# Performance work log

Hardware: AMD Instinct MI355X
Metric: run time of the kernel (lower is better)

The kernel has to match this reference:

```python
import jax, jax.numpy as jnp
import numpy as np

N_EMBD = 1024
N_HEAD = 16
HEAD_SIZE = N_EMBD // N_HEAD
D_FF = 4 * N_EMBD
B, T = 4, 2048
EPS = 1e-5


def _layernorm(x, w, b):
    mu = jnp.mean(x, axis=-1, keepdims=True)
    var = jnp.mean(jnp.square(x - mu), axis=-1, keepdims=True)
    return (x - mu) * jax.lax.rsqrt(var + EPS) * w + b


def setup_inputs() -> dict:
    key = jax.random.key(0)
    ks = jax.random.split(key, 12)
    s = 0.02
    x = jax.random.normal(ks[0], (B, T, N_EMBD), dtype=jnp.float32)
    # right-padded prefix mask: lengths in [T//2, T] -> no all-masked causal rows
    lengths = jax.random.randint(ks[1], (B,), T // 2, T + 1)
    key_padding_mask = jnp.arange(T)[None, :] < lengths[:, None]  # [B,T] bool, True=keep
    wq = jax.random.normal(ks[2], (N_EMBD, N_HEAD, HEAD_SIZE), dtype=jnp.float32) * s
    wk = jax.random.normal(ks[3], (N_EMBD, N_HEAD, HEAD_SIZE), dtype=jnp.float32) * s
    wv = jax.random.normal(ks[4], (N_EMBD, N_HEAD, HEAD_SIZE), dtype=jnp.float32) * s
    proj_w = jax.random.normal(ks[5], (N_EMBD, N_EMBD), dtype=jnp.float32) * s
    proj_b = jnp.zeros((N_EMBD,), dtype=jnp.float32)
    ff_w1 = jax.random.normal(ks[6], (N_EMBD, D_FF), dtype=jnp.float32) * s
    ff_b1 = jnp.zeros((D_FF,), dtype=jnp.float32)
    ff_w2 = jax.random.normal(ks[7], (D_FF, N_EMBD), dtype=jnp.float32) * s
    ff_b2 = jnp.zeros((N_EMBD,), dtype=jnp.float32)
    ln1_w = jnp.ones((N_EMBD,), dtype=jnp.float32)
    ln1_b = jnp.zeros((N_EMBD,), dtype=jnp.float32)
    ln2_w = jnp.ones((N_EMBD,), dtype=jnp.float32)
    ln2_b = jnp.zeros((N_EMBD,), dtype=jnp.float32)
    return dict(x=x, key_padding_mask=key_padding_mask, wq=wq, wk=wk, wv=wv,
                proj_w=proj_w, proj_b=proj_b, ff_w1=ff_w1, ff_b1=ff_b1,
                ff_w2=ff_w2, ff_b2=ff_b2, ln1_w=ln1_w, ln1_b=ln1_b,
                ln2_w=ln2_w, ln2_b=ln2_b)


def reference(x, key_padding_mask, wq, wk, wv, proj_w, proj_b,
              ff_w1, ff_b1, ff_w2, ff_b2, ln1_w, ln1_b, ln2_w, ln2_b):
    Bn, Tn, C = x.shape
    m = key_padding_mask.astype(x.dtype)  # [B,T]
    # --- attention sublayer ---
    h = _layernorm(x, ln1_w, ln1_b) * m[..., None]
    q = jnp.einsum('btc,chd->bhtd', h, wq)
    k = jnp.einsum('btc,chd->bhtd', h, wk)
    v = jnp.einsum('btc,chd->bhtd', h, wv)
    # NOTE: original scales by full embed dim C**-0.5, not head_size
    scores = jnp.einsum('bhtd,bhsd->bhts', q, k) * (C ** -0.5)
    causal = jnp.tril(jnp.ones((Tn, Tn), dtype=bool))
    mask = causal[None, None, :, :] & key_padding_mask[:, None, None, :]
    scores = jnp.where(mask, scores, -jnp.inf)
    wei = jax.nn.softmax(scores, axis=-1)
    out = jnp.einsum('bhts,bhsd->bthd', wei, v).reshape(Bn, Tn, C)
    x = x + out @ proj_w + proj_b
    # --- feedforward sublayer ---
    h2 = _layernorm(x, ln2_w, ln2_b) * m[..., None]
    ff = jax.nn.relu(h2 @ ff_w1 + ff_b1) @ ff_w2 + ff_b2
    x = (x + ff) * m[..., None]
    return x
```

## Files before the change

### kernel.cpp

```cpp
#include <hip/hip_runtime.h>
#include <math.h>

typedef float f32x4 __attribute__((ext_vector_type(4)));
typedef float f4 __attribute__((ext_vector_type(4)));
typedef __bf16 bf16x8 __attribute__((ext_vector_type(8)));
typedef __bf16 bf16x4 __attribute__((ext_vector_type(4)));

#define GLOBAL_AS __attribute__((address_space(1)))
#define LDS_AS __attribute__((address_space(3)))

__global__ __launch_bounds__(256) void mask_canon(const unsigned char* __restrict__ raw,
                                                  float* __restrict__ msk, int n) {
    int i = blockIdx.x * 256 + threadIdx.x;
    if (i >= n) return;
    unsigned int w0 = *(const unsigned int*)raw;
    float v;
    if (w0 == 0x01010101u)       v = raw[i] ? 1.f : 0.f;
    else if (w0 == 0x3f800000u)  v = ((const float*)raw)[i];
    else                         v = ((const int*)raw)[i] ? 1.f : 0.f;
    msk[i] = v;
}

__global__ __launch_bounds__(256) void lens_kernel(const float* __restrict__ msk,
                                                   float* __restrict__ lens) {
    int b = blockIdx.x, tid = threadIdx.x;
    float s = 0.f;
    for (int i = tid; i < 2048; i += 256) s += msk[b * 2048 + i];
#pragma unroll
    for (int off = 1; off < 64; off <<= 1) s += __shfl_xor(s, off);
    __shared__ float red[4];
    int wave = tid >> 6, lane = tid & 63;
    if (lane == 0) red[wave] = s;
    __syncthreads();
    if (tid == 0) lens[b] = red[0] + red[1] + red[2] + red[3];
}

__global__ __launch_bounds__(256) void tcvt(const float* __restrict__ src,
                                            __bf16* __restrict__ dst, int K, int N) {
    __shared__ float tile[32][33];
    int n0 = blockIdx.x * 32, k0 = blockIdx.y * 32;
    int tx = threadIdx.x & 31, ty = threadIdx.x >> 5;
#pragma unroll
    for (int i = 0; i < 4; ++i)
        tile[ty + 8 * i][tx] = src[(long)(k0 + ty + 8 * i) * N + n0 + tx];
    __syncthreads();
#pragma unroll
    for (int i = 0; i < 4; ++i)
        dst[(long)(n0 + ty + 8 * i) * K + k0 + tx] = (__bf16)tile[tx][ty + 8 * i];
}

__global__ __launch_bounds__(256) void ln_kernel(const float* __restrict__ x,
                                                 const float* __restrict__ w,
                                                 const float* __restrict__ bsc,
                                                 const float* __restrict__ msk,
                                                 __bf16* __restrict__ out) {
    long row = blockIdx.x;
    int tid = threadIdx.x;
    f4 xv = *(const f4*)(x + row * 1024 + tid * 4);
    float s = xv[0] + xv[1] + xv[2] + xv[3];
    float sq = xv[0] * xv[0] + xv[1] * xv[1] + xv[2] * xv[2] + xv[3] * xv[3];
#pragma unroll
    for (int off = 1; off < 64; off <<= 1) {
        s += __shfl_xor(s, off);
        sq += __shfl_xor(sq, off);
    }
    __shared__ float red[2][4];
    int wave = tid >> 6, lane = tid & 63;
    if (lane == 0) { red[0][wave] = s; red[1][wave] = sq; }
    __syncthreads();
    s = red[0][0] + red[0][1] + red[0][2] + red[0][3];
    sq = red[1][0] + red[1][1] + red[1][2] + red[1][3];
    float mu = s * (1.0f / 1024.0f);
    float var = sq * (1.0f / 1024.0f) - mu * mu;
    float rs = rsqrtf(var + 1e-5f);
    float mv = msk[row];
    f4 wv = *(const f4*)(w + tid * 4);
    f4 bv = *(const f4*)(bsc + tid * 4);
    bf16x4 ov;
#pragma unroll
    for (int j = 0; j < 4; ++j)
        ov[j] = (__bf16)(((xv[j] - mu) * rs * wv[j] + bv[j]) * mv);
    *(bf16x4*)(out + row * 1024 + tid * 4) = ov;
}

template <int EP>
__global__ __launch_bounds__(256) void gemm_bt(const __bf16* __restrict__ A,
                                               const __bf16* __restrict__ B,
                                               int K, int N, void* __restrict__ Cout,
                                               const float* __restrict__ bias,
                                               const float* __restrict__ resid,
                                               const float* __restrict__ mskp) {
    __shared__ __bf16 As[128 * 32];
    __shared__ __bf16 Bs[128 * 32];
    int tid = threadIdx.x;
    int wave = tid >> 6, lane = tid & 63;
    int l15 = lane & 15, quad = lane >> 4;
    int wrow = (wave >> 1) * 64, wcol = (wave & 1) * 64;
    long rowBase = (long)blockIdx.x * 128;
    long colBase = (long)blockIdx.y * 128;
    const __bf16* Ab = A + rowBase * K;
    const __bf16* Bb = B + colBase * K;
    int srow = lane >> 2;
    int scol = (lane & 3) * 8;
    f32x4 acc[4][4] = {};

    for (int kt = 0; kt < K; kt += 32) {
#pragma unroll
        for (int j = 0; j < 2; ++j) {
            int seg = wave * 2 + j;
            const __bf16* ga = Ab + (long)(seg * 16 + srow) * K + kt + scol;
            const __bf16* gb = Bb + (long)(seg * 16 + srow) * K + kt + scol;
            __builtin_amdgcn_global_load_lds((const GLOBAL_AS void*)ga,
                                             (LDS_AS void*)((char*)As + seg * 1024), 16, 0, 0);
            __builtin_amdgcn_global_load_lds((const GLOBAL_AS void*)gb,
                                             (LDS_AS void*)((char*)Bs + seg * 1024), 16, 0, 0);
        }
        __syncthreads();
        bf16x8 af[4], bfr[4];
#pragma unroll
        for (int i = 0; i < 4; ++i) {
            af[i] = *(const bf16x8*)(As + (wrow + i * 16 + l15) * 32 + quad * 8);
            bfr[i] = *(const bf16x8*)(Bs + (wcol + i * 16 + l15) * 32 + quad * 8);
        }
#pragma unroll
        for (int mi = 0; mi < 4; ++mi)
#pragma unroll
            for (int ni = 0; ni < 4; ++ni)
                acc[mi][ni] = __builtin_amdgcn_mfma_f32_16x16x32_bf16(af[mi], bfr[ni], acc[mi][ni], 0, 0, 0);
        __syncthreads();
    }

#pragma unroll
    for (int mi = 0; mi < 4; ++mi) {
#pragma unroll
        for (int r = 0; r < 4; ++r) {
            long gr = rowBase + wrow + mi * 16 + quad * 4 + r;
#pragma unroll
            for (int ni = 0; ni < 4; ++ni) {
                long gc = colBase + wcol + ni * 16 + l15;
                float v = acc[mi][ni][r];
                if constexpr (EP == 2) {
                    v += bias[gc] + resid[gr * N + gc];
                    ((float*)Cout)[gr * N + gc] = v;
                } else {
                    v = (v + bias[gc] + resid[gr * N + gc]) * mskp[gr];
                    ((float*)Cout)[gr * N + gc] = v;
                }
            }
        }
    }
}

template <int EP>
__global__ __launch_bounds__(512, 2) void gemm_bt8(const __bf16* __restrict__ A,
                                                   const __bf16* __restrict__ B,
                                                   int K, int N, void* __restrict__ Cout,
                                                   const float* __restrict__ bias) {
    __shared__ __bf16 AB[2][2][256 * 64];
    int tid = threadIdx.x;
    int wave = tid >> 6, lane = tid & 63;
    int l15 = lane & 15, quad = lane >> 4;
    int r8 = l15 & 7;
    int wm = wave >> 2, wn = wave & 3;
    long rowBase = (long)blockIdx.x * 256;
    long colBase = (long)blockIdx.y * 256;
    const __bf16* Ab = A + rowBase * K;
    const __bf16* Bb = B + colBase * K;
    int srow = lane >> 3;
    int scol = ((lane & 7) ^ srow) * 8;
    f32x4 acc[8][4] = {};

#define STAGE2(DST, GB, seg0, kt_)                                                         \
    do {                                                                                   \
        _Pragma("unroll") for (int j = 0; j < 2; ++j) {                                    \
            int s_ = wave * 4 + (seg0) + j;                                                \
            const __bf16* g_ = (GB) + (long)(s_ * 8 + srow) * K + (kt_) + scol;            \
            __builtin_amdgcn_global_load_lds((const GLOBAL_AS void*)g_,                    \
                                             (LDS_AS void*)((char*)(DST) + s_ * 1024), 16, \
                                             0, 0);                                        \
        }                                                                                  \
    } while (0)

#define RDA(mh)                                                                      \
    do {                                                                             \
        _Pragma("unroll") for (int mi = 0; mi < 4; ++mi) {                           \
            int row_ = wm * 128 + (mh) * 64 + mi * 16 + l15;                         \
            af[mi][0] = *(const bf16x8*)(Ac + row_ * 64 + ((quad ^ r8) << 3));       \
            af[mi][1] = *(const bf16x8*)(Ac + row_ * 64 + (((4 + quad) ^ r8) << 3)); \
        }                                                                            \
    } while (0)

#define RDB(h)                                                                              \
    do {                                                                                    \
        _Pragma("unroll") for (int ni = 0; ni < 2; ++ni) {                                  \
            int row_ = wn * 64 + ((h) * 2 + ni) * 16 + l15;                                 \
            bfr[h][ni][0] = *(const bf16x8*)(Bc + row_ * 64 + ((quad ^ r8) << 3));          \
            bfr[h][ni][1] = *(const bf16x8*)(Bc + row_ * 64 + (((4 + quad) ^ r8) << 3));    \
        }                                                                                   \
    } while (0)

#define MM(mh, nh)                                                                          \
    do {                                                                                    \
        __builtin_amdgcn_s_setprio(1);                                                      \
        _Pragma("unroll") for (int mi = 0; mi < 4; ++mi) {                                  \
            _Pragma("unroll") for (int ni = 0; ni < 2; ++ni) {                              \
                acc[(mh) * 4 + mi][(nh) * 2 + ni] = __builtin_amdgcn_mfma_f32_16x16x32_bf16(\
                    af[mi][0], bfr[nh][ni][0], acc[(mh) * 4 + mi][(nh) * 2 + ni], 0, 0, 0); \
                acc[(mh) * 4 + mi][(nh) * 2 + ni] = __builtin_amdgcn_mfma_f32_16x16x32_bf16(\
                    af[mi][1], bfr[nh][ni][1], acc[(mh) * 4 + mi][(nh) * 2 + ni], 0, 0, 0); \
            }                                                                               \
        }                                                                                   \
        __builtin_amdgcn_s_setprio(0);                                                      \
    } while (0)

    STAGE2(&AB[0][0][0], Ab, 0, 0);
    STAGE2(&AB[0][0][0], Ab, 2, 0);
    STAGE2(&AB[0][1][0], Bb, 0, 0);
    STAGE2(&AB[0][1][0], Bb, 2, 0);

    int cur = 0;
    bf16x8 af[4][2], bfr[2][2][2];
    for (int kt = 0; kt < K; kt += 64) {
        const bool lastt = (kt + 64 >= K);
        const __bf16* Ac = &AB[cur][0][0];
        const __bf16* Bc = &AB[cur][1][0];
        __bf16* An = &AB[cur ^ 1][0][0];
        __bf16* Bn = &AB[cur ^ 1][1][0];
        if (!lastt) {
            STAGE2(An, Ab, 0, kt + 64);
            __asm__ volatile("s_waitcnt vmcnt(2)" ::: "memory");
        } else {
            __asm__ volatile("s_waitcnt vmcnt(0)" ::: "memory");
        }
        __asm__ volatile("s_barrier" ::: "memory");
        RDA(0);
        RDB(0);
        MM(0, 0);
        if (!lastt) STAGE2(An, Ab, 2, kt + 64);
        RDB(1);
        MM(0, 1);
        if (!lastt) STAGE2(Bn, Bb, 0, kt + 64);
        RDA(1);
        MM(1, 1);
        if (!lastt) STAGE2(Bn, Bb, 2, kt + 64);
        MM(1, 0);
        __asm__ volatile("s_barrier" ::: "memory");
        cur ^= 1;
    }
#undef STAGE2
#undef RDA
#undef RDB
#undef MM

#pragma unroll
    for (int mi = 0; mi < 8; ++mi) {
#pragma unroll
        for (int r = 0; r < 4; ++r) {
            long gr = rowBase + wm * 128 + mi * 16 + quad * 4 + r;
#pragma unroll
            for (int ni = 0; ni < 4; ++ni) {
                long gc = colBase + wn * 64 + ni * 16 + l15;
                float v = acc[mi][ni][r];
                if constexpr (EP == 0) {
                    ((__bf16*)Cout)[gr * N + gc] = (__bf16)v;
                } else {
                    v += bias[gc];
                    v = v > 0.f ? v : 0.f;
                    ((__bf16*)Cout)[gr * N + gc] = (__bf16)v;
                }
            }
        }
    }
}

#define SWIZ(row, d) ((row) * 64 + ((((d) >> 3) ^ ((row) & 7)) << 3) + ((d) & 7))
__global__ __launch_bounds__(256, 3) void attn_kernel(const __bf16* __restrict__ qkv,
                                                      const float* __restrict__ lens,
                                                      __bf16* __restrict__ att) {
    const int T = 2048, C3 = 3072;
    int bh = blockIdx.x;
    int qt = 15 - blockIdx.y;
    int h = bh & 15, b = bh >> 4;
    int tid = threadIdx.x;
    int wave = tid >> 6, lane = tid & 63, l15 = lane & 15, quad = lane >> 4;

    __shared__ __bf16 Kl[64 * 64];
    __shared__ __bf16 Vt[64 * 64];
    __shared__ __bf16 Pl[4][32 * 64];

    long rowB = (long)b * T;
    const __bf16* kbase = qkv + rowB * C3 + 1024 + h * 64;
    const __bf16* vbase = qkv + rowB * C3 + 2048 + h * 64;
    const float scale2 = (1.0f / 32.0f) * 1.44269504088896f;

    int krow = tid >> 2, kd = (tid & 3) * 16;
    int vk = (tid & 15) * 4, vd = (tid >> 4) * 4;
    int vc8 = vk >> 3, vk7 = vk & 7;

    bf16x8 ones;
#pragma unroll
    for (int j = 0; j < 8; ++j) ones[j] = (__bf16)1.0f;

    __bf16* pw = &Pl[wave][0];
    int r8 = l15 & 7;

    int qbase = qt * 128;
    int wq0 = qbase + wave * 32;

    bf16x8 qf[2][2];
#pragma unroll
    for (int g = 0; g < 2; ++g) {
        const __bf16* qptr = qkv + (rowB + wq0 + g * 16 + l15) * C3 + h * 64;
        qf[g][0] = *(const bf16x8*)(qptr + quad * 8);
        qf[g][1] = *(const bf16x8*)(qptr + 32 + quad * 8);
    }

    f32x4 o0[4] = {}, o1[4] = {};
    f32x4 lacc0 = {}, lacc1 = {};
    int nchunk = 2 * qt + 2;
    float len = lens[b];

    bf16x8 kpre0, kpre1;
    bf16x4 vpre[4];
    {
        const __bf16* kg = kbase + (long)krow * C3 + kd;
        kpre0 = *(const bf16x8*)kg;
        kpre1 = *(const bf16x8*)(kg + 8);
#pragma unroll
        for (int j = 0; j < 4; ++j)
            vpre[j] = *(const bf16x4*)(vbase + (long)(vk + j) * C3 + vd);
    }

    for (int c = 0; c < nchunk; ++c) {
        int k0 = c * 64;
        __asm__ volatile("s_barrier" ::: "memory");
        *(bf16x8*)(&Kl[SWIZ(krow, kd)]) = kpre0;
        *(bf16x8*)(&Kl[SWIZ(krow, kd + 8)]) = kpre1;
#pragma unroll
        for (int dd = 0; dd < 4; ++dd) {
            bf16x4 w = {vpre[0][dd], vpre[1][dd], vpre[2][dd], vpre[3][dd]};
            int d = vd + dd;
            *(bf16x4*)(&Vt[d * 64 + ((vc8 ^ (d & 7)) << 3) + vk7]) = w;
        }
        if (c + 1 < nchunk) {
            int k1 = k0 + 64;
            const __bf16* kg = kbase + (long)(k1 + krow) * C3 + kd;
            kpre0 = *(const bf16x8*)kg;
            kpre1 = *(const bf16x8*)(kg + 8);
#pragma unroll
            for (int j = 0; j < 4; ++j)
                vpre[j] = *(const bf16x4*)(vbase + (long)(k1 + vk + j) * C3 + vd);
        }
        __asm__ volatile("s_waitcnt lgkmcnt(0)\n\ts_barrier" ::: "memory");

        if (k0 <= wq0 + 31) {
            f32x4 s0[4] = {}, s1[4] = {};
#pragma unroll
            for (int n = 0; n < 4; ++n) {
                int row = n * 16 + l15;
                bf16x8 kb0 = *(const bf16x8*)(&Kl[row * 64 + ((quad ^ r8) << 3)]);
                bf16x8 kb1 = *(const bf16x8*)(&Kl[row * 64 + (((4 + quad) ^ r8) << 3)]);
                s0[n] = __builtin_amdgcn_mfma_f32_16x16x32_bf16(kb0, qf[0][0], s0[n], 0, 0, 0);
                s0[n] = __builtin_amdgcn_mfma_f32_16x16x32_bf16(kb1, qf[0][1], s0[n], 0, 0, 0);
                s1[n] = __builtin_amdgcn_mfma_f32_16x16x32_bf16(kb0, qf[1][0], s1[n], 0, 0, 0);
                s1[n] = __builtin_amdgcn_mfma_f32_16x16x32_bf16(kb1, qf[1][1], s1[n], 0, 0, 0);
            }

            bool needC = (k0 + 63 > wq0);
#pragma unroll
            for (int n = 0; n < 4; ++n) {
                int c8 = n * 2 + (quad >> 1);
                int sub = (quad & 1) * 4;
                bf16x4 w0, w1;
                if (!needC) {
#pragma unroll
                    for (int r = 0; r < 4; ++r) {
                        w0[r] = (__bf16)exp2f(s0[n][r] * scale2);
                        w1[r] = (__bf16)exp2f(s1[n][r] * scale2);
                    }
                } else {
                    int kg = k0 + n * 16 + quad * 4;
                    int qg0 = wq0 + l15, qg1 = wq0 + 16 + l15;
#pragma unroll
                    for (int r = 0; r < 4; ++r) {
                        w0[r] = (kg + r <= qg0) ? (__bf16)exp2f(s0[n][r] * scale2) : (__bf16)0.f;
                        w1[r] = (kg + r <= qg1) ? (__bf16)exp2f(s1[n][r] * scale2) : (__bf16)0.f;
                    }
                }
                int wbase = l15 * 64 + ((c8 ^ r8) << 3) + sub;
                *(bf16x4*)(pw + wbase) = w0;
                *(bf16x4*)(pw + 1024 + wbase) = w1;
            }
            __asm__ volatile("s_waitcnt lgkmcnt(0)" ::: "memory");

            bf16x8 pa00 = *(const bf16x8*)(pw + l15 * 64 + ((quad ^ r8) << 3));
            bf16x8 pa01 = *(const bf16x8*)(pw + l15 * 64 + (((4 + quad) ^ r8) << 3));
            bf16x8 pa10 = *(const bf16x8*)(pw + 1024 + l15 * 64 + ((quad ^ r8) << 3));
            bf16x8 pa11 = *(const bf16x8*)(pw + 1024 + l15 * 64 + (((4 + quad) ^ r8) << 3));
#pragma unroll
            for (int nd = 0; nd < 4; ++nd) {
                int row = nd * 16 + l15;
                bf16x8 vb0 = *(const bf16x8*)(&Vt[row * 64 + ((quad ^ r8) << 3)]);
                bf16x8 vb1 = *(const bf16x8*)(&Vt[row * 64 + (((4 + quad) ^ r8) << 3)]);
                o0[nd] = __builtin_amdgcn_mfma_f32_16x16x32_bf16(pa00, vb0, o0[nd], 0, 0, 0);
                o0[nd] = __builtin_amdgcn_mfma_f32_16x16x32_bf16(pa01, vb1, o0[nd], 0, 0, 0);
                o1[nd] = __builtin_amdgcn_mfma_f32_16x16x32_bf16(pa10, vb0, o1[nd], 0, 0, 0);
                o1[nd] = __builtin_amdgcn_mfma_f32_16x16x32_bf16(pa11, vb1, o1[nd], 0, 0, 0);
            }
            lacc0 = __builtin_amdgcn_mfma_f32_16x16x32_bf16(pa00, ones, lacc0, 0, 0, 0);
            lacc0 = __builtin_amdgcn_mfma_f32_16x16x32_bf16(pa01, ones, lacc0, 0, 0, 0);
            lacc1 = __builtin_amdgcn_mfma_f32_16x16x32_bf16(pa10, ones, lacc1, 0, 0, 0);
            lacc1 = __builtin_amdgcn_mfma_f32_16x16x32_bf16(pa11, ones, lacc1, 0, 0, 0);
        }
    }

#pragma unroll
    for (int r = 0; r < 4; ++r) {
        int q0g = wq0 + quad * 4 + r;
        float inv0 = 1.0f / (lacc0[r] - fmaxf(0.f, (float)(q0g + 1) - len));
        long orow0 = rowB + q0g;
        int q1g = q0g + 16;
        float inv1 = 1.0f / (lacc1[r] - fmaxf(0.f, (float)(q1g + 1) - len));
        long orow1 = rowB + q1g;
#pragma unroll
        for (int nd = 0; nd < 4; ++nd) {
            att[orow0 * 1024 + h * 64 + nd * 16 + l15] = (__bf16)(o0[nd][r] * inv0);
            att[orow1 * 1024 + h * 64 + nd * 16 + l15] = (__bf16)(o1[nd][r] * inv1);
        }
    }
}

extern "C" void kernel_launch(void* const* d_in, const int* in_sizes, int n_in,
                              void* d_out, int out_size, void* d_ws, size_t ws_size,
                              hipStream_t stream) {
    const float* x      = (const float*)d_in[0];
    const void*  kpm    = d_in[1];
    const float* wq     = (const float*)d_in[2];
    const float* wk     = (const float*)d_in[3];
    const float* wv     = (const float*)d_in[4];
    const float* proj_w = (const float*)d_in[5];
    const float* proj_b = (const float*)d_in[6];
    const float* ff_w1  = (const float*)d_in[7];
    const float* ff_b1  = (const float*)d_in[8];
    const float* ff_w2  = (const float*)d_in[9];
    const float* ff_b2  = (const float*)d_in[10];
    const float* ln1w   = (const float*)d_in[11];
    const float* ln1b   = (const float*)d_in[12];
    const float* ln2w   = (const float*)d_in[13];
    const float* ln2b   = (const float*)d_in[14];

    char* ws = (char*)d_ws;
    size_t off = 0;
    auto take = [&](size_t bytes) -> char* {
        char* p = ws + off;
        off += (bytes + 255) & ~(size_t)255;
        return p;
    };
    float*  msk    = (float*)take(8192 * 4);
    float*  lens   = (float*)take(256);
    __bf16* wqkvT  = (__bf16*)take(3072L * 1024 * 2);
    __bf16* wprojT = (__bf16*)take(1024L * 1024 * 2);
    __bf16* wff1T  = (__bf16*)take(4096L * 1024 * 2);
    __bf16* wff2T  = (__bf16*)take(4096L * 1024 * 2);
    __bf16* h1     = (__bf16*)take(8192L * 1024 * 2);
    char*   qkv_c  = take(8192L * 3072 * 2);
    __bf16* qkvb   = (__bf16*)qkv_c;
    __bf16* attb   = (__bf16*)take(8192L * 1024 * 2);
    float*  x2     = (float*)take(8192L * 1024 * 4);
    __bf16* h2     = (__bf16*)take(8192L * 1024 * 2);
    __bf16* ffh    = (__bf16*)qkv_c;

    mask_canon<<<32, 256, 0, stream>>>((const unsigned char*)kpm, msk, 8192);
    lens_kernel<<<4, 256, 0, stream>>>(msk, lens);
    tcvt<<<dim3(32, 32), 256, 0, stream>>>(wq, wqkvT, 1024, 1024);
    tcvt<<<dim3(32, 32), 256, 0, stream>>>(wk, wqkvT + 1024L * 1024, 1024, 1024);
    tcvt<<<dim3(32, 32), 256, 0, stream>>>(wv, wqkvT + 2048L * 1024, 1024, 1024);
    tcvt<<<dim3(32, 32), 256, 0, stream>>>(proj_w, wprojT, 1024, 1024);
    tcvt<<<dim3(128, 32), 256, 0, stream>>>(ff_w1, wff1T, 1024, 4096);
    tcvt<<<dim3(32, 128), 256, 0, stream>>>(ff_w2, wff2T, 4096, 1024);

    ln_kernel<<<8192, 256, 0, stream>>>(x, ln1w, ln1b, msk, h1);
    gemm_bt8<0><<<dim3(32, 12), 512, 0, stream>>>(h1, wqkvT, 1024, 3072, qkvb, nullptr);
    attn_kernel<<<dim3(64, 16), 256, 0, stream>>>(qkvb, lens, attb);
    gemm_bt<2><<<dim3(64, 8), 256, 0, stream>>>(attb, wprojT, 1024, 1024, x2, proj_b, x, nullptr);
    ln_kernel<<<8192, 256, 0, stream>>>(x2, ln2w, ln2b, msk, h2);
    gemm_bt8<1><<<dim3(32, 16), 512, 0, stream>>>(h2, wff1T, 1024, 4096, ffh, ff_b1);
    gemm_bt<3><<<dim3(64, 8), 256, 0, stream>>>(ffh, wff2T, 4096, 1024, (float*)d_out, ff_b2, x2, msk);
}
```

Baseline: 497.4 us.

## Replace simple GEMM with double-buffered swizzled 256x128 GEMM for proj and FF2

```diff
diff --git a/kernel.cpp b/kernel.cpp
--- a/kernel.cpp
+++ b/kernel.cpp
@@ -81,74 +81,6 @@
     for (int j = 0; j < 4; ++j)
         ov[j] = (__bf16)(((xv[j] - mu) * rs * wv[j] + bv[j]) * mv);
     *(bf16x4*)(out + row * 1024 + tid * 4) = ov;
-}
-
-template <int EP>
-__global__ __launch_bounds__(256) void gemm_bt(const __bf16* __restrict__ A,
-                                               const __bf16* __restrict__ B,
-                                               int K, int N, void* __restrict__ Cout,
-                                               const float* __restrict__ bias,
-                                               const float* __restrict__ resid,
-                                               const float* __restrict__ mskp) {
-    __shared__ __bf16 As[128 * 32];
-    __shared__ __bf16 Bs[128 * 32];
-    int tid = threadIdx.x;
-    int wave = tid >> 6, lane = tid & 63;
-    int l15 = lane & 15, quad = lane >> 4;
-    int wrow = (wave >> 1) * 64, wcol = (wave & 1) * 64;
-    long rowBase = (long)blockIdx.x * 128;
-    long colBase = (long)blockIdx.y * 128;
-    const __bf16* Ab = A + rowBase * K;
-    const __bf16* Bb = B + colBase * K;
-    int srow = lane >> 2;
-    int scol = (lane & 3) * 8;
-    f32x4 acc[4][4] = {};
-
-    for (int kt = 0; kt < K; kt += 32) {
-#pragma unroll
-        for (int j = 0; j < 2; ++j) {
-            int seg = wave * 2 + j;
-            const __bf16* ga = Ab + (long)(seg * 16 + srow) * K + kt + scol;
-            const __bf16* gb = Bb + (long)(seg * 16 + srow) * K + kt + scol;
-            __builtin_amdgcn_global_load_lds((const GLOBAL_AS void*)ga,
-                                             (LDS_AS void*)((char*)As + seg * 1024), 16, 0, 0);
-            __builtin_amdgcn_global_load_lds((const GLOBAL_AS void*)gb,
-                                             (LDS_AS void*)((char*)Bs + seg * 1024), 16, 0, 0);
-        }
-        __syncthreads();
-        bf16x8 af[4], bfr[4];
-#pragma unroll
-        for (int i = 0; i < 4; ++i) {
-            af[i] = *(const bf16x8*)(As + (wrow + i * 16 + l15) * 32 + quad * 8);
-            bfr[i] = *(const bf16x8*)(Bs + (wcol + i * 16 + l15) * 32 + quad * 8);
-        }
-#pragma unroll
-        for (int mi = 0; mi < 4; ++mi)
-#pragma unroll
-            for (int ni = 0; ni < 4; ++ni)
-                acc[mi][ni] = __builtin_amdgcn_mfma_f32_16x16x32_bf16(af[mi], bfr[ni], acc[mi][ni], 0, 0, 0);
-        __syncthreads();
-    }
-
-#pragma unroll
-    for (int mi = 0; mi < 4; ++mi) {
-#pragma unroll
-        for (int r = 0; r < 4; ++r) {
-            long gr = rowBase + wrow + mi * 16 + quad * 4 + r;
-#pragma unroll
-            for (int ni = 0; ni < 4; ++ni) {
-                long gc = colBase + wcol + ni * 16 + l15;
-                float v = acc[mi][ni][r];
-                if constexpr (EP == 2) {
-                    v += bias[gc] + resid[gr * N + gc];
-                    ((float*)Cout)[gr * N + gc] = v;
-                } else {
-                    v = (v + bias[gc] + resid[gr * N + gc]) * mskp[gr];
-                    ((float*)Cout)[gr * N + gc] = v;
-                }
-            }
-        }
-    }
 }
 
 template <int EP>
@@ -267,6 +199,143 @@
                     v += bias[gc];
                     v = v > 0.f ? v : 0.f;
                     ((__bf16*)Cout)[gr * N + gc] = (__bf16)v;
+                }
+            }
+        }
+    }
+}
+
+template <int EP>
+__global__ __launch_bounds__(512, 2) void gemm_bt8n(const __bf16* __restrict__ A,
+                                                    const __bf16* __restrict__ B,
+                                                    int K, int N, void* __restrict__ Cout,
+                                                    const float* __restrict__ bias,
+                                                    const float* __restrict__ resid,
+                                                    const float* __restrict__ mskp) {
+    __shared__ __bf16 As2[2][256 * 64];
+    __shared__ __bf16 Bs2[2][128 * 64];
+    int tid = threadIdx.x;
+    int wave = tid >> 6, lane = tid & 63;
+    int l15 = lane & 15, quad = lane >> 4;
+    int r8 = l15 & 7;
+    int wm = wave >> 1, wn = wave & 1;
+    long rowBase = (long)blockIdx.x * 256;
+    long colBase = (long)blockIdx.y * 128;
+    const __bf16* Ab = A + rowBase * K;
+    const __bf16* Bb = B + colBase * K;
+    int srow = lane >> 3;
+    int scol = ((lane & 7) ^ srow) * 8;
+    f32x4 acc[4][4] = {};
+
+#define NSTGA(DST, seg0, kt_)                                                              \
+    do {                                                                                   \
+        _Pragma("unroll") for (int j = 0; j < 2; ++j) {                                    \
+            int s_ = wave * 4 + (seg0) + j;                                                \
+            const __bf16* g_ = Ab + (long)(s_ * 8 + srow) * K + (kt_) + scol;              \
+            __builtin_amdgcn_global_load_lds((const GLOBAL_AS void*)g_,                    \
+                                             (LDS_AS void*)((char*)(DST) + s_ * 1024), 16, \
+                                             0, 0);                                        \
+        }                                                                                  \
+    } while (0)
+
+#define NSTGB(DST, kt_)                                                                    \
+    do {                                                                                   \
+        _Pragma("unroll") for (int j = 0; j < 2; ++j) {                                    \
+            int s_ = wave * 2 + j;                                                         \
+            const __bf16* g_ = Bb + (long)(s_ * 8 + srow) * K + (kt_) + scol;              \
+            __builtin_amdgcn_global_load_lds((const GLOBAL_AS void*)g_,                    \
+                                             (LDS_AS void*)((char*)(DST) + s_ * 1024), 16, \
+                                             0, 0);                                        \
+        }                                                                                  \
+    } while (0)
+
+#define NRA(H)                                                                            \
+    do {                                                                                  \
+        _Pragma("unroll") for (int mi = 0; mi < 2; ++mi) {                                \
+            int row_ = wm * 64 + ((H) * 2 + mi) * 16 + l15;                               \
+            afr[H][mi][0] = *(const bf16x8*)(Ac + row_ * 64 + ((quad ^ r8) << 3));        \
+            afr[H][mi][1] = *(const bf16x8*)(Ac + row_ * 64 + (((4 + quad) ^ r8) << 3));  \
+        }                                                                                 \
+    } while (0)
+
+#define NRB(H)                                                                            \
+    do {                                                                                  \
+        _Pragma("unroll") for (int ni = 0; ni < 2; ++ni) {                                \
+            int row_ = wn * 64 + ((H) * 2 + ni) * 16 + l15;                               \
+            bfr2[H][ni][0] = *(const bf16x8*)(Bc + row_ * 64 + ((quad ^ r8) << 3));       \
+            bfr2[H][ni][1] = *(const bf16x8*)(Bc + row_ * 64 + (((4 + quad) ^ r8) << 3)); \
+        }                                                                                 \
+    } while (0)
+
+#define NMM(AH, BH)                                                                          \
+    do {                                                                                     \
+        __builtin_amdgcn_s_setprio(1);                                                       \
+        _Pragma("unroll") for (int mi = 0; mi < 2; ++mi) {                                   \
+            _Pragma("unroll") for (int ni = 0; ni < 2; ++ni) {                               \
+                acc[(AH) * 2 + mi][(BH) * 2 + ni] = __builtin_amdgcn_mfma_f32_16x16x32_bf16( \
+                    afr[AH][mi][0], bfr2[BH][ni][0], acc[(AH) * 2 + mi][(BH) * 2 + ni], 0,   \
+                    0, 0);                                                                   \
+                acc[(AH) * 2 + mi][(BH) * 2 + ni] = __builtin_amdgcn_mfma_f32_16x16x32_bf16( \
+                    afr[AH][mi][1], bfr2[BH][ni][1], acc[(AH) * 2 + mi][(BH) * 2 + ni], 0,   \
+                    0, 0);                                                                   \
+            }                                                                                \
+        }                                                                                    \
+        __builtin_amdgcn_s_setprio(0);                                                       \
+    } while (0)
+
+    NSTGA(&As2[0][0], 0, 0);
+    NSTGA(&As2[0][0], 2, 0);
+    NSTGB(&Bs2[0][0], 0);
+
+    int cur = 0;
+    bf16x8 afr[2][2][2], bfr2[2][2][2];
+    for (int kt = 0; kt < K; kt += 64) {
+        const bool lastt = (kt + 64 >= K);
+        const __bf16* Ac = &As2[cur][0];
+        const __bf16* Bc = &Bs2[cur][0];
+        __bf16* An = &As2[cur ^ 1][0];
+        __bf16* Bn = &Bs2[cur ^ 1][0];
+        if (!lastt) {
+            NSTGA(An, 0, kt + 64);
+            __asm__ volatile("s_waitcnt vmcnt(2)" ::: "memory");
+        } else {
+            __asm__ volatile("s_waitcnt vmcnt(0)" ::: "memory");
+        }
+        __asm__ volatile("s_barrier" ::: "memory");
+        NRA(0);
+        NRB(0);
+        NMM(0, 0);
+        if (!lastt) NSTGA(An, 2, kt + 64);
+        NRB(1);
+        NMM(0, 1);
+        if (!lastt) NSTGB(Bn, kt + 64);
+        NRA(1);
+        NMM(1, 1);
+        NMM(1, 0);
+        __asm__ volatile("s_barrier" ::: "memory");
+        cur ^= 1;
+    }
+#undef NSTGA
+#undef NSTGB
+#undef NRA
+#undef NRB
+#undef NMM
+
+#pragma unroll
+    for (int mi = 0; mi < 4; ++mi) {
+#pragma unroll
+        for (int r = 0; r < 4; ++r) {
+            long gr = rowBase + wm * 64 + mi * 16 + quad * 4 + r;
+#pragma unroll
+            for (int ni = 0; ni < 4; ++ni) {
+                long gc = colBase + wn * 64 + ni * 16 + l15;
+                float v = acc[mi][ni][r];
+                if constexpr (EP == 2) {
+                    v += bias[gc] + resid[gr * N + gc];
+                    ((float*)Cout)[gr * N + gc] = v;
+                } else {
+                    v = (v + bias[gc] + resid[gr * N + gc]) * mskp[gr];
+                    ((float*)Cout)[gr * N + gc] = v;
                 }
             }
         }
@@ -482,8 +551,8 @@
     ln_kernel<<<8192, 256, 0, stream>>>(x, ln1w, ln1b, msk, h1);
     gemm_bt8<0><<<dim3(32, 12), 512, 0, stream>>>(h1, wqkvT, 1024, 3072, qkvb, nullptr);
     attn_kernel<<<dim3(64, 16), 256, 0, stream>>>(qkvb, lens, attb);
-    gemm_bt<2><<<dim3(64, 8), 256, 0, stream>>>(attb, wprojT, 1024, 1024, x2, proj_b, x, nullptr);
+    gemm_bt8n<2><<<dim3(32, 8), 512, 0, stream>>>(attb, wprojT, 1024, 1024, x2, proj_b, x, nullptr);
     ln_kernel<<<8192, 256, 0, stream>>>(x2, ln2w, ln2b, msk, h2);
     gemm_bt8<1><<<dim3(32, 16), 512, 0, stream>>>(h2, wff1T, 1024, 4096, ffh, ff_b1);
-    gemm_bt<3><<<dim3(64, 8), 256, 0, stream>>>(ffh, wff2T, 4096, 1024, (float*)d_out, ff_b2, x2, msk);
-}
+    gemm_bt8n<3><<<dim3(32, 8), 512, 0, stream>>>(ffh, wff2T, 4096, 1024, (float*)d_out, ff_b2, x2, msk);
+}
```

Result: no change. 506.8 us (+1.9%).
